# Performance work log

Hardware: AMD Instinct MI355X
Metric: run time of the kernel (lower is better)

Reference implementation:

```python
import jax, jax.numpy as jnp
import numpy as np

MAX_RAY_LENGTH = 200.0


def setup_inputs() -> dict:
    key = jax.random.key(0)
    ks = jax.random.split(key, 6)
    D, K, R = 1296, 64, 16          # num_directions, num_points, rank
    F = 408                          # num_subcarriers
    return {
        "attenuation_real": jax.random.normal(ks[0], (D, K, R), dtype=jnp.float32),
        "attenuation_imag": jax.random.normal(ks[1], (D, K, R), dtype=jnp.float32),
        "radiation_real": jax.random.normal(ks[2], (D, K, R), dtype=jnp.float32),
        "radiation_imag": jax.random.normal(ks[3], (D, K, R), dtype=jnp.float32),
        "freq_real": jax.random.normal(ks[4], (F, R), dtype=jnp.float32),
        "freq_imag": jax.random.normal(ks[5], (F, R), dtype=jnp.float32),
    }


def reference(attenuation_real, attenuation_imag, radiation_real, radiation_imag,
              freq_real, freq_imag):
    # Complexify (complex64)
    att = jax.lax.complex(attenuation_real, attenuation_imag)   # (D, K, R)
    rad = jax.lax.complex(radiation_real, radiation_imag)       # (D, K, R)
    fbv = jax.lax.complex(freq_real, freq_imag)                 # (F, R)

    num_directions, num_points, _ = att.shape
    delta_t = MAX_RAY_LENGTH / num_points

    # u_hat_rho = cumsum over points of conj(att) * delta_t  (D, K, R)
    u_hat_rho = jnp.cumsum(jnp.conj(att) * delta_t, axis=1)

    # Factorized equivalent of the original rank^2 / rank^3 outer-product einsums:
    # einsum('rki,rkj->rkij', rad*, att*) contracted with einsum('fi,fj->fij', f, f)
    # == (rad* @ f^T) * (att* @ f^T) summed over i,j separately.
    p = jnp.einsum('rki,fi->rkf', jnp.conj(rad), fbv)           # (D, K, F)
    q = jnp.einsum('rki,fi->rkf', jnp.conj(att), fbv)           # (D, K, F)

    first_order = (p * q).sum(axis=1) * delta_t                  # (D, F)

    # Second order uses points [1:] and conj(u_hat_rho)
    h = jnp.einsum('rkl,fl->rkf', jnp.conj(u_hat_rho), fbv)     # (D, K, F)
    second_order = (p[:, 1:] * q[:, 1:] * h[:, 1:]).sum(axis=1) * delta_t  # (D, F)

    csi = (first_order + second_order).sum(axis=0) / num_directions  # (F,)
    return csi
```

## Files before the change

kernel.cpp:

```cpp
#include <hip/hip_runtime.h>

#define D_DIRS 1296
#define K_PTS  64
#define R_RANK 16
#define F_SUB  408
#define DT_VAL (200.0f / 64.0f)

#define NBLOCKS (D_DIRS / 2)
#define PARTIAL_FLOATS 8704
#define RED_CHUNKS 12
#define SLABS_PER_CHUNK (NBLOCKS / RED_CHUNKS)
#define NEED_BYTES ((size_t)(1 + RED_CHUNKS + NBLOCKS) * PARTIAL_FLOATS * 4)

union alignas(16) SMem {
    struct { float2 att[2][K_PTS * R_RANK]; float2 rad[2][K_PTS * R_RANK]; } tiles;
    float red[PARTIAL_FLOATS];
};

template <bool USE_PARTIALS>
__global__ __launch_bounds__(512) void accum_kernel_t(
    const float* __restrict__ att_r, const float* __restrict__ att_i,
    const float* __restrict__ rad_r, const float* __restrict__ rad_i,
    float* __restrict__ T_ws, float* __restrict__ pbuf)
{
    __shared__ SMem sm;

    const int t  = threadIdx.x;
    const int h  = t >> 8;
    const int t2 = t & 255;
    const int ri = t2 >> 4;
    const int rj = t2 & 15;
    const int d  = blockIdx.x * 2 + h;
    const int base = d * K_PTS * R_RANK;

    float2* sA = sm.tiles.att[h];
    float2* sR = sm.tiles.rad[h];
#pragma unroll
    for (int v = t2; v < K_PTS * R_RANK; v += 256) {
        sA[v] = make_float2(att_r[base + v], att_i[base + v]);
        sR[v] = make_float2(rad_r[base + v], rad_i[base + v]);
    }
    __syncthreads();

    float accR[16], accI[16];
#pragma unroll
    for (int l = 0; l < 16; ++l) { accR[l] = 0.f; accI[l] = 0.f; }
    float Sr = 0.f, Si = 0.f;

    for (int k = K_PTS - 1; k >= 1; --k) {
        float2 a = sR[k * 16 + ri];
        float2 b = sA[k * 16 + rj];
        Sr += a.x * b.x - a.y * b.y;
        Si -= a.x * b.y + a.y * b.x;
#pragma unroll
        for (int q = 0; q < 8; ++q) {
            float4 c = *reinterpret_cast<const float4*>(&sA[k * 16 + q * 2]);
            accR[q * 2]     += Sr * c.x - Si * c.y;
            accI[q * 2]     += Sr * c.y + Si * c.x;
            accR[q * 2 + 1] += Sr * c.z - Si * c.w;
            accI[q * 2 + 1] += Sr * c.w + Si * c.z;
        }
    }
#pragma unroll
    for (int q = 0; q < 8; ++q) {
        float4 c = *reinterpret_cast<const float4*>(&sA[q * 2]);
        accR[q * 2]     += Sr * c.x - Si * c.y;
        accI[q * 2]     += Sr * c.y + Si * c.x;
        accR[q * 2 + 1] += Sr * c.z - Si * c.w;
        accI[q * 2 + 1] += Sr * c.w + Si * c.z;
    }
    float2 a0 = sR[ri], b0 = sA[rj];
    float gR = Sr + (a0.x * b0.x - a0.y * b0.y);
    float gI = Si - (a0.x * b0.y + a0.y * b0.x);

    __syncthreads();
    if (h == 1) {
        float4* r4 = (float4*)sm.red;
#pragma unroll
        for (int q = 0; q < 8; ++q) {
            r4[t2 * 8 + (q ^ (t2 & 7))] =
                make_float4(accR[q * 2], accI[q * 2], accR[q * 2 + 1], accI[q * 2 + 1]);
        }
        sm.red[8192 + t2 * 2 + 0] = gR;
        sm.red[8192 + t2 * 2 + 1] = gI;
    }
    __syncthreads();
    if (h == 0) {
        if (USE_PARTIALS) {
            float4* slabT = (float4*)(pbuf + (size_t)blockIdx.x * PARTIAL_FLOATS);
            const float4* r4 = (const float4*)sm.red;
#pragma unroll
            for (int q = 0; q < 8; ++q) {
                float4 o = r4[t2 * 8 + (q ^ (t2 & 7))];
                slabT[t2 * 8 + q] = make_float4(
                    (accR[q * 2]     + o.x) * DT_VAL, (accI[q * 2]     + o.y) * DT_VAL,
                    (accR[q * 2 + 1] + o.z) * DT_VAL, (accI[q * 2 + 1] + o.w) * DT_VAL);
            }
            float2* slabG = (float2*)(pbuf + (size_t)blockIdx.x * PARTIAL_FLOATS + 8192);
            slabG[t2] = make_float2(gR + sm.red[8192 + t2 * 2],
                                    gI + sm.red[8192 + t2 * 2 + 1]);
        } else {
            const float4* r4 = (const float4*)sm.red;
#pragma unroll
            for (int q = 0; q < 8; ++q) {
                float4 o = r4[t2 * 8 + (q ^ (t2 & 7))];
                atomicAdd(&T_ws[(t2 * 8 + q) * 4 + 0], (accR[q * 2]     + o.x) * DT_VAL);
                atomicAdd(&T_ws[(t2 * 8 + q) * 4 + 1], (accI[q * 2]     + o.y) * DT_VAL);
                atomicAdd(&T_ws[(t2 * 8 + q) * 4 + 2], (accR[q * 2 + 1] + o.z) * DT_VAL);
                atomicAdd(&T_ws[(t2 * 8 + q) * 4 + 3], (accI[q * 2 + 1] + o.w) * DT_VAL);
            }
            atomicAdd(&T_ws[8192 + t2 * 2 + 0], gR + sm.red[8192 + t2 * 2]);
            atomicAdd(&T_ws[8192 + t2 * 2 + 1], gI + sm.red[8192 + t2 * 2 + 1]);
        }
    }
}

__global__ __launch_bounds__(256) void reduce1_kernel(
    const float* __restrict__ pbuf, float* __restrict__ red1)
{
    int e = blockIdx.x * 256 + threadIdx.x;
    float s = 0.f;
    const float* p = pbuf + (size_t)blockIdx.y * SLABS_PER_CHUNK * PARTIAL_FLOATS + e;
#pragma unroll 6
    for (int b = 0; b < SLABS_PER_CHUNK; ++b)
        s += p[(size_t)b * PARTIAL_FLOATS];
    red1[blockIdx.y * PARTIAL_FLOATS + e] = s;
}

__global__ __launch_bounds__(256) void reduce2_kernel(
    const float* __restrict__ red1, float* __restrict__ TG_out)
{
    int e = blockIdx.x * 256 + threadIdx.x;
    float s = 0.f;
#pragma unroll
    for (int c = 0; c < RED_CHUNKS; ++c)
        s += red1[c * PARTIAL_FLOATS + e];
    TG_out[e] = s;
}

__global__ __launch_bounds__(256) void contract_kernel(
    const float* __restrict__ fr, const float* __restrict__ fi,
    const float* __restrict__ T_ws, const float* __restrict__ G_ws,
    float* __restrict__ out)
{
    const int f = blockIdx.x;
    const int t = threadIdx.x;
    const int i = t >> 4;
    const int j = t & 15;

    __shared__ float sfr[16], sfi[16];
    if (t < 16) {
        sfr[t] = fr[f * R_RANK + t];
        sfi[t] = fi[f * R_RANK + t];
    }
    __syncthreads();

    float fir = sfr[i], fii = sfi[i];
    float fjr = sfr[j], fji = sfi[j];
    float mr = fir * fjr - fii * fji;
    float mi = fir * fji + fii * fjr;

    float Sr = G_ws[t * 2 + 0];
    float Si = G_ws[t * 2 + 1];
#pragma unroll
    for (int l = 0; l < 16; ++l) {
        float Tr = T_ws[(t * 16 + l) * 2 + 0];
        float Ti = T_ws[(t * 16 + l) * 2 + 1];
        float flr = sfr[l], fli = sfi[l];
        Sr += Tr * flr - Ti * fli;
        Si += Tr * fli + Ti * flr;
    }

    float vr = Sr * mr - Si * mi;
    float vi = Sr * mi + Si * mr;

#pragma unroll
    for (int off = 32; off >= 1; off >>= 1) {
        vr += __shfl_down(vr, off, 64);
        vi += __shfl_down(vi, off, 64);
    }
    __shared__ float red[8];
    const int lane = t & 63, w = t >> 6;
    if (lane == 0) { red[w * 2] = vr; red[w * 2 + 1] = vi; }
    __syncthreads();
    if (t == 0) {
        float rr = red[0] + red[2] + red[4] + red[6];
        float ii = red[1] + red[3] + red[5] + red[7];
        const float scale = DT_VAL / (float)D_DIRS;
        out[f]         = rr * scale;
        out[F_SUB + f] = ii * scale;
    }
}

extern "C" void kernel_launch(void* const* d_in, const int* in_sizes, int n_in,
                              void* d_out, int out_size, void* d_ws, size_t ws_size,
                              hipStream_t stream)
{
    const float* att_r = (const float*)d_in[0];
    const float* att_i = (const float*)d_in[1];
    const float* rad_r = (const float*)d_in[2];
    const float* rad_i = (const float*)d_in[3];
    const float* fr    = (const float*)d_in[4];
    const float* fi    = (const float*)d_in[5];

    float* ws   = (float*)d_ws;
    float* T_ws = ws;
    float* G_ws = ws + 8192;
    float* red1 = ws + PARTIAL_FLOATS;
    float* pbuf = ws + (1 + RED_CHUNKS) * PARTIAL_FLOATS;

    const bool use_partials = ws_size >= NEED_BYTES;

    if (use_partials) {
        accum_kernel_t<true><<<NBLOCKS, 512, 0, stream>>>(
            att_r, att_i, rad_r, rad_i, T_ws, pbuf);
        reduce1_kernel<<<dim3(PARTIAL_FLOATS / 256, RED_CHUNKS), 256, 0, stream>>>(
            pbuf, red1);
        reduce2_kernel<<<PARTIAL_FLOATS / 256, 256, 0, stream>>>(red1, T_ws);
    } else {
        hipMemsetAsync(T_ws, 0, PARTIAL_FLOATS * sizeof(float), stream);
        accum_kernel_t<false><<<NBLOCKS, 512, 0, stream>>>(
            att_r, att_i, rad_r, rad_i, T_ws, pbuf);
    }

    contract_kernel<<<F_SUB, 256, 0, stream>>>(
        fr, fi, T_ws, G_ws, (float*)d_out);
}
```

Before: 167.1 us.

## Process two directions per 256-thread block and fuse final reduction into contract

The accumulation kernel now uses 256 threads that loop over both directions in sequence and keep the sum in registers. This removes the shared-memory cross-half reduction and its extra barriers, and launch bounds now request higher occupancy. The second reduction kernel is dropped. Each contract block instead sums the 12 chunk partials into skewed shared memory, which saves one launch but repeats that reduction in all 408 blocks. Serialising the two directions doubles the per-thread dependent loop length.

```diff
diff --git a/kernel.cpp b/kernel.cpp
--- a/kernel.cpp
+++ b/kernel.cpp
@@ -10,108 +10,93 @@
 #define PARTIAL_FLOATS 8704
 #define RED_CHUNKS 12
 #define SLABS_PER_CHUNK (NBLOCKS / RED_CHUNKS)
-#define NEED_BYTES ((size_t)(1 + RED_CHUNKS + NBLOCKS) * PARTIAL_FLOATS * 4)
-
-union alignas(16) SMem {
-    struct { float2 att[2][K_PTS * R_RANK]; float2 rad[2][K_PTS * R_RANK]; } tiles;
-    float red[PARTIAL_FLOATS];
-};
+#define NEED_BYTES ((size_t)(RED_CHUNKS + NBLOCKS) * PARTIAL_FLOATS * 4)
+#define SKEW(e) ((e) + ((e) >> 5))
 
 template <bool USE_PARTIALS>
-__global__ __launch_bounds__(512) void accum_kernel_t(
+__global__ __launch_bounds__(256, 4) void accum_kernel_t(
     const float* __restrict__ att_r, const float* __restrict__ att_i,
     const float* __restrict__ rad_r, const float* __restrict__ rad_i,
-    float* __restrict__ T_ws, float* __restrict__ pbuf)
-{
-    __shared__ SMem sm;
+    float* __restrict__ pbuf, float* __restrict__ atomic_dst)
+{
+    __shared__ float4 sAtt4[2][K_PTS * 8];
+    __shared__ float2 sRad2[2][K_PTS * R_RANK];
 
     const int t  = threadIdx.x;
-    const int h  = t >> 8;
-    const int t2 = t & 255;
-    const int ri = t2 >> 4;
-    const int rj = t2 & 15;
-    const int d  = blockIdx.x * 2 + h;
-    const int base = d * K_PTS * R_RANK;
-
-    float2* sA = sm.tiles.att[h];
-    float2* sR = sm.tiles.rad[h];
-#pragma unroll
-    for (int v = t2; v < K_PTS * R_RANK; v += 256) {
-        sA[v] = make_float2(att_r[base + v], att_i[base + v]);
-        sR[v] = make_float2(rad_r[base + v], rad_i[base + v]);
+    const int ri = t >> 4;
+    const int rj = t & 15;
+
+    for (int h = 0; h < 2; ++h) {
+        const int base = (blockIdx.x * 2 + h) * K_PTS * R_RANK;
+#pragma unroll
+        for (int s = t; s < 512; s += 256) {
+            float2 ar = *(const float2*)(att_r + base + 2 * s);
+            float2 ai = *(const float2*)(att_i + base + 2 * s);
+            sAtt4[h][s] = make_float4(ar.x, ai.x, ar.y, ai.y);
+            float2 rr = *(const float2*)(rad_r + base + 2 * s);
+            float2 rim = *(const float2*)(rad_i + base + 2 * s);
+            sRad2[h][2 * s]     = make_float2(rr.x, rim.x);
+            sRad2[h][2 * s + 1] = make_float2(rr.y, rim.y);
+        }
     }
     __syncthreads();
 
     float accR[16], accI[16];
 #pragma unroll
     for (int l = 0; l < 16; ++l) { accR[l] = 0.f; accI[l] = 0.f; }
-    float Sr = 0.f, Si = 0.f;
-
-    for (int k = K_PTS - 1; k >= 1; --k) {
-        float2 a = sR[k * 16 + ri];
-        float2 b = sA[k * 16 + rj];
-        Sr += a.x * b.x - a.y * b.y;
-        Si -= a.x * b.y + a.y * b.x;
+    float gR = 0.f, gI = 0.f;
+
+    for (int h = 0; h < 2; ++h) {
+        const float2* rad2 = sRad2[h];
+        const float2* att2 = (const float2*)sAtt4[h];
+        const float4* att4 = sAtt4[h];
+
+        float Sr = 0.f, Si = 0.f;
+        for (int k = K_PTS - 1; k >= 1; --k) {
+            float2 a = rad2[k * 16 + ri];
+            float2 b = att2[k * 16 + rj];
+            Sr += a.x * b.x - a.y * b.y;
+            Si -= a.x * b.y + a.y * b.x;
+#pragma unroll
+            for (int q = 0; q < 8; ++q) {
+                float4 c = att4[k * 8 + q];
+                accR[2 * q]     += Sr * c.x - Si * c.y;
+                accI[2 * q]     += Sr * c.y + Si * c.x;
+                accR[2 * q + 1] += Sr * c.z - Si * c.w;
+                accI[2 * q + 1] += Sr * c.w + Si * c.z;
+            }
+        }
 #pragma unroll
         for (int q = 0; q < 8; ++q) {
-            float4 c = *reinterpret_cast<const float4*>(&sA[k * 16 + q * 2]);
-            accR[q * 2]     += Sr * c.x - Si * c.y;
-            accI[q * 2]     += Sr * c.y + Si * c.x;
-            accR[q * 2 + 1] += Sr * c.z - Si * c.w;
-            accI[q * 2 + 1] += Sr * c.w + Si * c.z;
-        }
-    }
-#pragma unroll
-    for (int q = 0; q < 8; ++q) {
-        float4 c = *reinterpret_cast<const float4*>(&sA[q * 2]);
-        accR[q * 2]     += Sr * c.x - Si * c.y;
-        accI[q * 2]     += Sr * c.y + Si * c.x;
-        accR[q * 2 + 1] += Sr * c.z - Si * c.w;
-        accI[q * 2 + 1] += Sr * c.w + Si * c.z;
-    }
-    float2 a0 = sR[ri], b0 = sA[rj];
-    float gR = Sr + (a0.x * b0.x - a0.y * b0.y);
-    float gI = Si - (a0.x * b0.y + a0.y * b0.x);
-
-    __syncthreads();
-    if (h == 1) {
-        float4* r4 = (float4*)sm.red;
-#pragma unroll
-        for (int q = 0; q < 8; ++q) {
-            r4[t2 * 8 + (q ^ (t2 & 7))] =
-                make_float4(accR[q * 2], accI[q * 2], accR[q * 2 + 1], accI[q * 2 + 1]);
-        }
-        sm.red[8192 + t2 * 2 + 0] = gR;
-        sm.red[8192 + t2 * 2 + 1] = gI;
-    }
-    __syncthreads();
-    if (h == 0) {
-        if (USE_PARTIALS) {
-            float4* slabT = (float4*)(pbuf + (size_t)blockIdx.x * PARTIAL_FLOATS);
-            const float4* r4 = (const float4*)sm.red;
-#pragma unroll
-            for (int q = 0; q < 8; ++q) {
-                float4 o = r4[t2 * 8 + (q ^ (t2 & 7))];
-                slabT[t2 * 8 + q] = make_float4(
-                    (accR[q * 2]     + o.x) * DT_VAL, (accI[q * 2]     + o.y) * DT_VAL,
-                    (accR[q * 2 + 1] + o.z) * DT_VAL, (accI[q * 2 + 1] + o.w) * DT_VAL);
-            }
-            float2* slabG = (float2*)(pbuf + (size_t)blockIdx.x * PARTIAL_FLOATS + 8192);
-            slabG[t2] = make_float2(gR + sm.red[8192 + t2 * 2],
-                                    gI + sm.red[8192 + t2 * 2 + 1]);
-        } else {
-            const float4* r4 = (const float4*)sm.red;
-#pragma unroll
-            for (int q = 0; q < 8; ++q) {
-                float4 o = r4[t2 * 8 + (q ^ (t2 & 7))];
-                atomicAdd(&T_ws[(t2 * 8 + q) * 4 + 0], (accR[q * 2]     + o.x) * DT_VAL);
-                atomicAdd(&T_ws[(t2 * 8 + q) * 4 + 1], (accI[q * 2]     + o.y) * DT_VAL);
-                atomicAdd(&T_ws[(t2 * 8 + q) * 4 + 2], (accR[q * 2 + 1] + o.z) * DT_VAL);
-                atomicAdd(&T_ws[(t2 * 8 + q) * 4 + 3], (accI[q * 2 + 1] + o.w) * DT_VAL);
-            }
-            atomicAdd(&T_ws[8192 + t2 * 2 + 0], gR + sm.red[8192 + t2 * 2]);
-            atomicAdd(&T_ws[8192 + t2 * 2 + 1], gI + sm.red[8192 + t2 * 2 + 1]);
-        }
+            float4 c = att4[q];
+            accR[2 * q]     += Sr * c.x - Si * c.y;
+            accI[2 * q]     += Sr * c.y + Si * c.x;
+            accR[2 * q + 1] += Sr * c.z - Si * c.w;
+            accI[2 * q + 1] += Sr * c.w + Si * c.z;
+        }
+        float2 a0 = rad2[ri], b0 = att2[rj];
+        gR += Sr + (a0.x * b0.x - a0.y * b0.y);
+        gI += Si - (a0.x * b0.y + a0.y * b0.x);
+    }
+
+    if (USE_PARTIALS) {
+        float4* slabT = (float4*)(pbuf + (size_t)blockIdx.x * PARTIAL_FLOATS);
+#pragma unroll
+        for (int v = 0; v < 8; ++v) {
+            slabT[t * 8 + v] = make_float4(
+                accR[2 * v] * DT_VAL,     accI[2 * v] * DT_VAL,
+                accR[2 * v + 1] * DT_VAL, accI[2 * v + 1] * DT_VAL);
+        }
+        float2* slabG = (float2*)(pbuf + (size_t)blockIdx.x * PARTIAL_FLOATS + 8192);
+        slabG[t] = make_float2(gR, gI);
+    } else {
+#pragma unroll
+        for (int l = 0; l < 16; ++l) {
+            atomicAdd(&atomic_dst[(t * 16 + l) * 2 + 0], accR[l] * DT_VAL);
+            atomicAdd(&atomic_dst[(t * 16 + l) * 2 + 1], accI[l] * DT_VAL);
+        }
+        atomicAdd(&atomic_dst[8192 + t * 2 + 0], gR);
+        atomicAdd(&atomic_dst[8192 + t * 2 + 1], gI);
     }
 }
 
@@ -119,53 +104,51 @@
     const float* __restrict__ pbuf, float* __restrict__ red1)
 {
     int e = blockIdx.x * 256 + threadIdx.x;
+    const float* p = pbuf + (size_t)blockIdx.y * SLABS_PER_CHUNK * PARTIAL_FLOATS + e;
     float s = 0.f;
-    const float* p = pbuf + (size_t)blockIdx.y * SLABS_PER_CHUNK * PARTIAL_FLOATS + e;
 #pragma unroll 6
     for (int b = 0; b < SLABS_PER_CHUNK; ++b)
         s += p[(size_t)b * PARTIAL_FLOATS];
     red1[blockIdx.y * PARTIAL_FLOATS + e] = s;
 }
 
-__global__ __launch_bounds__(256) void reduce2_kernel(
-    const float* __restrict__ red1, float* __restrict__ TG_out)
-{
-    int e = blockIdx.x * 256 + threadIdx.x;
-    float s = 0.f;
-#pragma unroll
-    for (int c = 0; c < RED_CHUNKS; ++c)
-        s += red1[c * PARTIAL_FLOATS + e];
-    TG_out[e] = s;
-}
-
 __global__ __launch_bounds__(256) void contract_kernel(
     const float* __restrict__ fr, const float* __restrict__ fi,
-    const float* __restrict__ T_ws, const float* __restrict__ G_ws,
-    float* __restrict__ out)
-{
+    const float* __restrict__ red1, float* __restrict__ out)
+{
+    __shared__ float sTG[PARTIAL_FLOATS + PARTIAL_FLOATS / 32];
+    __shared__ float sfr[16], sfi[16];
+
     const int f = blockIdx.x;
     const int t = threadIdx.x;
-    const int i = t >> 4;
-    const int j = t & 15;
-
-    __shared__ float sfr[16], sfi[16];
+
+    for (int e = t; e < PARTIAL_FLOATS; e += 256) {
+        float s = 0.f;
+#pragma unroll
+        for (int c = 0; c < RED_CHUNKS; ++c)
+            s += red1[c * PARTIAL_FLOATS + e];
+        sTG[SKEW(e)] = s;
+    }
     if (t < 16) {
         sfr[t] = fr[f * R_RANK + t];
         sfi[t] = fi[f * R_RANK + t];
     }
     __syncthreads();
 
+    const int i = t >> 4, j = t & 15;
     float fir = sfr[i], fii = sfi[i];
     float fjr = sfr[j], fji = sfi[j];
     float mr = fir * fjr - fii * fji;
     float mi = fir * fji + fii * fjr;
 
-    float Sr = G_ws[t * 2 + 0];
-    float Si = G_ws[t * 2 + 1];
+    int gbase = 8192 + t * 2;
+    float Sr = sTG[SKEW(gbase)];
+    float Si = sTG[SKEW(gbase + 1)];
 #pragma unroll
     for (int l = 0; l < 16; ++l) {
-        float Tr = T_ws[(t * 16 + l) * 2 + 0];
-        float Ti = T_ws[(t * 16 + l) * 2 + 1];
+        int e0 = (t * 16 + l) * 2;
+        float Tr = sTG[SKEW(e0)];
+        float Ti = sTG[SKEW(e0 + 1)];
         float flr = sfr[l], fli = sfi[l];
         Sr += Tr * flr - Ti * fli;
         Si += Tr * fli + Ti * flr;
@@ -204,25 +187,22 @@
     const float* fi    = (const float*)d_in[5];
 
     float* ws   = (float*)d_ws;
-    float* T_ws = ws;
-    float* G_ws = ws + 8192;
-    float* red1 = ws + PARTIAL_FLOATS;
-    float* pbuf = ws + (1 + RED_CHUNKS) * PARTIAL_FLOATS;
+    float* red1 = ws;
+    float* pbuf = ws + RED_CHUNKS * PARTIAL_FLOATS;
 
     const bool use_partials = ws_size >= NEED_BYTES;
 
     if (use_partials) {
-        accum_kernel_t<true><<<NBLOCKS, 512, 0, stream>>>(
-            att_r, att_i, rad_r, rad_i, T_ws, pbuf);
+        accum_kernel_t<true><<<NBLOCKS, 256, 0, stream>>>(
+            att_r, att_i, rad_r, rad_i, pbuf, red1);
         reduce1_kernel<<<dim3(PARTIAL_FLOATS / 256, RED_CHUNKS), 256, 0, stream>>>(
             pbuf, red1);
-        reduce2_kernel<<<PARTIAL_FLOATS / 256, 256, 0, stream>>>(red1, T_ws);
     } else {
-        hipMemsetAsync(T_ws, 0, PARTIAL_FLOATS * sizeof(float), stream);
-        accum_kernel_t<false><<<NBLOCKS, 512, 0, stream>>>(
-            att_r, att_i, rad_r, rad_i, T_ws, pbuf);
+        hipMemsetAsync(red1, 0, RED_CHUNKS * PARTIAL_FLOATS * sizeof(float), stream);
+        accum_kernel_t<false><<<NBLOCKS, 256, 0, stream>>>(
+            att_r, att_i, rad_r, rad_i, pbuf, red1);
     }
 
     contract_kernel<<<F_SUB, 256, 0, stream>>>(
-        fr, fi, T_ws, G_ws, (float*)d_out);
-}
+        fr, fi, red1, (float*)d_out);
+}
```

Result: no change. 168.7 us (+1.0%).
